# Optimization experiments

Hardware: AMD Instinct MI355X
Metric: run time of the kernel (lower is better)

## Reference

```python
import jax, jax.numpy as jnp
import numpy as np

B, L, D = 4, 2048, 512   # batch, seq_len, model_dim
H, A = 8, 64             # head_num, atten_dim (H*A == D)
EPS = 1e-5


def setup_inputs() -> dict:
    key = jax.random.key(0)
    ks = jax.random.split(key, 20)
    std = 1.0 / np.sqrt(D)
    inp = {}
    for i, name in enumerate(["Q_data", "Q_time", "K_data", "K_time", "V_time"]):
        inp[name] = jax.random.normal(ks[i], (B, L, D), dtype=jnp.float32)
    # projection params (torch Linear: y = x @ W.T + b); store as [in, out]
    for i, name in enumerate(["Wq_d", "Wq_t", "Wk_d", "Wk_t", "Wv_t", "Wo"]):
        inp[name + "_w"] = jax.random.uniform(ks[5 + i], (D, H * A), jnp.float32, -std, std)
        inp[name + "_b"] = jax.random.uniform(ks[11 + i], (H * A,), jnp.float32, -std, std)
    inp["ln_g"] = jnp.ones((D,), jnp.float32)
    inp["ln_b"] = jnp.zeros((D,), jnp.float32)
    return inp


def _proj(x, w, b):
    # [B,L,D] -> [B,H,L,A]
    y = jnp.einsum('bld,de->ble', x, w) + b
    return y.reshape(B, L, H, A).transpose(0, 2, 1, 3)


def reference(Q_data, Q_time, K_data, K_time, V_time,
              Wq_d_w, Wq_t_w, Wk_d_w, Wk_t_w, Wv_t_w, Wo_w,
              Wq_d_b, Wq_t_b, Wk_d_b, Wk_t_b, Wv_t_b, Wo_b,
              ln_g, ln_b):
    residual = Q_data
    qd = _proj(Q_data, Wq_d_w, Wq_d_b)
    qt = _proj(Q_time, Wq_t_w, Wq_t_b)
    kd = _proj(K_data, Wk_d_w, Wk_d_b)
    kt = _proj(K_time, Wk_t_w, Wk_t_b)
    vt = _proj(V_time, Wv_t_w, Wv_t_b)
    scale = 1.0 / np.sqrt(A)
    # dual QK^T scores summed before softmax
    scores = (jnp.einsum('bhqa,bhka->bhqk', qd, kd)
              + jnp.einsum('bhqa,bhka->bhqk', qt, kt)) * scale
    attn = jax.nn.softmax(scores, axis=-1)
    ctx = jnp.einsum('bhqk,bhka->bhqa', attn, vt)        # [B,H,L,A]
    ctx = ctx.transpose(0, 2, 1, 3).reshape(B, L, H * A)  # [B,L,D]
    out = jnp.einsum('bld,de->ble', ctx, Wo_w) + Wo_b
    x = out + residual
    mu = jnp.mean(x, axis=-1, keepdims=True)
    var = jnp.var(x, axis=-1, keepdims=True)
    return (x - mu) / jnp.sqrt(var + EPS) * ln_g + ln_b
```

## Files before the change

### kernel.cpp

```cpp
#include <hip/hip_runtime.h>
#include <hip/hip_bf16.h>
#include <stdint.h>


using f32x4  = __attribute__((ext_vector_type(4))) float;
using bf16x8 = __attribute__((ext_vector_type(8))) short;

typedef __attribute__((address_space(1))) const uint32_t g_u32;
typedef __attribute__((address_space(3))) uint32_t l_u32;

#if __has_builtin(__builtin_amdgcn_exp2f)
#define EXP2F __builtin_amdgcn_exp2f
#else
#define EXP2F exp2f
#endif
#define QSCALE 0.1803368801111204f

__device__ __forceinline__ void glds16(const void* g, void* l) {
  __builtin_amdgcn_global_load_lds((g_u32*)g, (l_u32*)l, 16, 0, 0);
}

__device__ __forceinline__ unsigned short f2bfu(float f) {
  __hip_bfloat16 h = __float2bfloat16(f);
  union { __hip_bfloat16 h; unsigned short u; } v;
  v.h = h;
  return v.u;
}

__device__ __forceinline__ uint32_t pack_trunc(float lo, float hi) {
  union { float f; uint32_t u; } a, b;
  a.f = lo; b.f = hi;
  return __builtin_amdgcn_perm(b.u, a.u, 0x07060302u);
}

__global__ __launch_bounds__(256) void k_prep_w(
    const float* __restrict__ w0, const float* __restrict__ w1,
    const float* __restrict__ w2, const float* __restrict__ w3,
    const float* __restrict__ w4, const float* __restrict__ w5,
    unsigned short* __restrict__ wt) {
  __shared__ float tile[64][68];
  const float* wsrc[6] = {w0, w1, w2, w3, w4, w5};
  int bid = blockIdx.x;
  int mat = bid >> 6, tid = bid & 63;
  int k0 = (tid >> 3) << 6, c0 = (tid & 7) << 6;
  const float* w = wsrc[mat];
  int t = threadIdx.x;
  {
    int r = t >> 2, cq = (t & 3) << 4;
    const float4* src = reinterpret_cast<const float4*>(w + (size_t)(k0 + r) * 512 + c0 + cq);
#pragma unroll
    for (int j = 0; j < 4; ++j) {
      float4 v = src[j];
      tile[r][cq + j * 4 + 0] = v.x;
      tile[r][cq + j * 4 + 1] = v.y;
      tile[r][cq + j * 4 + 2] = v.z;
      tile[r][cq + j * 4 + 3] = v.w;
    }
  }
  __syncthreads();
  {
    int cc = t >> 2, kq = (t & 3) << 4;
    union { unsigned short u[16]; uint4 v[2]; } p;
#pragma unroll
    for (int j = 0; j < 16; ++j) p.u[j] = f2bfu(tile[kq + j][cc]);
    unsigned short* dst = wt + (size_t)mat * 262144 + (size_t)(c0 + cc) * 512 + k0 + kq;
    *reinterpret_cast<uint4*>(dst)     = p.v[0];
    *reinterpret_cast<uint4*>(dst + 8) = p.v[1];
  }
}

__global__ __launch_bounds__(512) void k_proj2(
    const float* __restrict__ x0, const float* __restrict__ x1,
    const float* __restrict__ x2, const float* __restrict__ x3,
    const float* __restrict__ x4,
    const unsigned short* __restrict__ wt,
    const float* __restrict__ b0, const float* __restrict__ b1,
    const float* __restrict__ b2, const float* __restrict__ b3,
    const float* __restrict__ b4,
    unsigned short* __restrict__ qws, unsigned short* __restrict__ kws,
    unsigned short* __restrict__ vws) {
  __shared__ __align__(16) unsigned short Abuf[8192];
  __shared__ __align__(16) unsigned short Bbuf[2][8192];
  int bid = blockIdx.x;
  int proj = bid >> 8, rem = bid & 255;
  int cb = rem >> 6, rb = rem & 63;
  const float* xs[5] = {x0, x1, x2, x3, x4};
  const float* Ag = xs[proj] + (size_t)rb * 128 * 512;
  const unsigned short* Wg = wt + (size_t)proj * 262144 + (size_t)cb * 128 * 512;
  int t = threadIdx.x;
  int lane = t & 63, w = t >> 6, wr = w >> 2, wc = w & 3, g = lane >> 4, c = lane & 15;
  f32x4 acc[4][2];
#pragma unroll
  for (int i = 0; i < 4; ++i)
#pragma unroll
    for (int j = 0; j < 2; ++j) acc[i][j] = f32x4{0.f, 0.f, 0.f, 0.f};

  int srow[2], sch[2];
#pragma unroll
  for (int j = 0; j < 2; ++j) {
    int q = t + j * 512;
    srow[j] = q >> 3;
    sch[j] = q & 7;
  }
  float4 pa[2], pb[2];
#pragma unroll
  for (int j = 0; j < 2; ++j) {
    const float* src = Ag + (size_t)srow[j] * 512 + sch[j] * 8;
    pa[j] = *reinterpret_cast<const float4*>(src);
    pb[j] = *reinterpret_cast<const float4*>(src + 4);
  }
#pragma unroll
  for (int j = 0; j < 2; ++j) {
    int cid = t + j * 512;
    int row = cid >> 3, ch = cid & 7;
    glds16(Wg + (size_t)row * 512 + ((ch ^ (row & 7)) << 3), &Bbuf[0][cid * 8]);
  }

#pragma unroll 1
  for (int it = 0; it < 8; ++it) {
    int cur = it & 1;
    __syncthreads();
#pragma unroll
    for (int j = 0; j < 2; ++j) {
      union { unsigned short u[8]; uint4 v; } p;
      p.u[0] = f2bfu(pa[j].x); p.u[1] = f2bfu(pa[j].y);
      p.u[2] = f2bfu(pa[j].z); p.u[3] = f2bfu(pa[j].w);
      p.u[4] = f2bfu(pb[j].x); p.u[5] = f2bfu(pb[j].y);
      p.u[6] = f2bfu(pb[j].z); p.u[7] = f2bfu(pb[j].w);
      *reinterpret_cast<uint4*>(&Abuf[srow[j] * 64 + ((sch[j] ^ (srow[j] & 7)) << 3)]) = p.v;
    }
    __syncthreads();
    if (it < 7) {
#pragma unroll
      for (int j = 0; j < 2; ++j) {
        const float* src = Ag + (size_t)srow[j] * 512 + (it + 1) * 64 + sch[j] * 8;
        pa[j] = *reinterpret_cast<const float4*>(src);
        pb[j] = *reinterpret_cast<const float4*>(src + 4);
      }
#pragma unroll
      for (int j = 0; j < 2; ++j) {
        int cid = t + j * 512;
        int row = cid >> 3, ch = cid & 7;
        glds16(Wg + (size_t)row * 512 + (it + 1) * 64 + ((ch ^ (row & 7)) << 3),
               &Bbuf[cur ^ 1][cid * 8]);
      }
    }
#pragma unroll
    for (int fi = 0; fi < 2; ++fi) {
      bf16x8 af[4], bfr[2];
#pragma unroll
      for (int mi = 0; mi < 4; ++mi) {
        int arow = wr * 64 + mi * 16 + c;
        af[mi] = *reinterpret_cast<const bf16x8*>(
            &Abuf[arow * 64 + (((fi * 4 + g) ^ (arow & 7)) << 3)]);
      }
#pragma unroll
      for (int ni = 0; ni < 2; ++ni) {
        int brow = wc * 32 + ni * 16 + c;
        bfr[ni] = *reinterpret_cast<const bf16x8*>(
            &Bbuf[cur][brow * 64 + (((fi * 4 + g) ^ (brow & 7)) << 3)]);
      }
      __builtin_amdgcn_s_setprio(1);
#pragma unroll
      for (int mi = 0; mi < 4; ++mi)
#pragma unroll
        for (int ni = 0; ni < 2; ++ni)
          acc[mi][ni] = __builtin_amdgcn_mfma_f32_16x16x32_bf16(af[mi], bfr[ni], acc[mi][ni], 0, 0, 0);
      __builtin_amdgcn_s_setprio(0);
    }
  }

  const float* bias_arr[5] = {b0, b1, b2, b3, b4};
  const float* bias = bias_arr[proj];
  float scale = (proj < 2) ? QSCALE : 1.0f;
  unsigned short* qkdst = (proj < 2) ? qws : kws;
  int half = (proj & 1) ? 64 : 0;
#pragma unroll
  for (int ni = 0; ni < 2; ++ni) {
    int n = wc * 32 + ni * 16 + c;
    int h = cb * 2 + (n >> 6);
    int a = n & 63;
    float bv = bias[cb * 128 + n];
#pragma unroll
    for (int mi = 0; mi < 4; ++mi) {
#pragma unroll
      for (int rr = 0; rr < 4; ++rr) {
        float v = (acc[mi][ni][rr] + bv) * scale;
        unsigned short u = f2bfu(v);
        int rowg = rb * 128 + wr * 64 + mi * 16 + g * 4 + rr;
        int b = rowg >> 11, l = rowg & 2047;
        if (proj < 4) {
          qkdst[((size_t)(b * 8 + h) * 2048 + l) * 128 + half + a] = u;
        } else {
          vws[((size_t)(b * 8 + h) * 64 + a) * 2048 + l] = u;
        }
      }
    }
  }
}

__device__ __forceinline__ void gemm_core(
    const unsigned short* Ag, const unsigned short* Wg,
    unsigned short* Al, unsigned short* Bl, f32x4 acc[4]) {
  int t = threadIdx.x;
  int lane = t & 63, w = t >> 6, g = lane >> 4, c = lane & 15;
#pragma unroll 1
  for (int it = 0; it < 8; ++it) {
    __syncthreads();
#pragma unroll
    for (int j = 0; j < 2; ++j) {
      int cid = t + j * 256;
      int row = cid >> 3, ch = cid & 7;
      glds16(Ag + (size_t)row * 512 + it * 64 + ((ch ^ (row & 7)) << 3), Al + cid * 8);
      glds16(Wg + (size_t)row * 512 + it * 64 + ((ch ^ (row & 7)) << 3), Bl + cid * 8);
    }
    __syncthreads();
#pragma unroll
    for (int fi = 0; fi < 2; ++fi) {
      int arow = w * 16 + c;
      bf16x8 af = *reinterpret_cast<const bf16x8*>(
          Al + arow * 64 + (((fi * 4 + g) ^ (arow & 7)) << 3));
#pragma unroll
      for (int ct = 0; ct < 4; ++ct) {
        int brow = ct * 16 + c;
        bf16x8 bf = *reinterpret_cast<const bf16x8*>(
            Bl + brow * 64 + (((fi * 4 + g) ^ (brow & 7)) << 3));
        acc[ct] = __builtin_amdgcn_mfma_f32_16x16x32_bf16(af, bf, acc[ct], 0, 0, 0);
      }
    }
  }
}

__global__ __launch_bounds__(256) void k_attn(
    const unsigned short* __restrict__ qws, const unsigned short* __restrict__ kws,
    const unsigned short* __restrict__ vws, unsigned short* __restrict__ ctxb) {
  __shared__ __align__(16) unsigned short Kb[2][8192];
  __shared__ __align__(16) unsigned short Vb[2][4096];
  __shared__ __align__(16) unsigned short Pl[4][2][1152];
  int orig = blockIdx.x;
  int xcd = orig & 7, j = orig >> 3;
  int bh = xcd * 4 + (j >> 4), qb = j & 15;
  int t = threadIdx.x;
  int w = t >> 6, lane = t & 63, g = lane >> 4, c = lane & 15;

  const unsigned short* Kg = kws + (size_t)bh * 2048 * 128;
  const unsigned short* Vg = vws + (size_t)bh * 64 * 2048;

  bf16x8 qf[2][4];
#pragma unroll
  for (int qt = 0; qt < 2; ++qt) {
    const unsigned short* Qg =
        qws + ((size_t)bh * 2048 + qb * 128 + w * 32 + qt * 16 + c) * 128;
#pragma unroll
    for (int fi = 0; fi < 4; ++fi)
      qf[qt][fi] = *reinterpret_cast<const bf16x8*>(Qg + fi * 32 + g * 8);
  }

  f32x4 o[2][4];
#pragma unroll
  for (int qt = 0; qt < 2; ++qt)
#pragma unroll
    for (int at = 0; at < 4; ++at) o[qt][at] = f32x4{0.f, 0.f, 0.f, 0.f};
  float lsum[2] = {0.f, 0.f};
  char* Pw0 = reinterpret_cast<char*>(&Pl[w][0][0]) + c * 144;
  char* Pw1 = reinterpret_cast<char*>(&Pl[w][1][0]) + c * 144;

#pragma unroll
  for (int jj = 0; jj < 4; ++jj) {
    int cid = t + jj * 256;
    int row = cid >> 4, ch = cid & 15;
    glds16(Kg + (size_t)row * 128 + ((ch ^ (row & 15)) << 3), &Kb[0][cid * 8]);
  }
#pragma unroll
  for (int jj = 0; jj < 2; ++jj) {
    int cid = t + jj * 256;
    int a = cid >> 3, ch = cid & 7;
    glds16(Vg + (size_t)a * 2048 + ((ch ^ (a & 7)) << 3), &Vb[0][cid * 8]);
  }
  __syncthreads();

#pragma unroll 1
  for (int it = 0; it < 32; ++it) {
    int cur = it & 1;
    if (it < 31) {
      int nxt = cur ^ 1;
#pragma unroll
      for (int jj = 0; jj < 4; ++jj) {
        int cid = t + jj * 256;
        int row = cid >> 4, ch = cid & 15;
        glds16(Kg + ((size_t)(it + 1) * 64 + row) * 128 + ((ch ^ (row & 15)) << 3),
               &Kb[nxt][cid * 8]);
      }
#pragma unroll
      for (int jj = 0; jj < 2; ++jj) {
        int cid = t + jj * 256;
        int a = cid >> 3, ch = cid & 7;
        glds16(Vg + (size_t)a * 2048 + (it + 1) * 64 + ((ch ^ (a & 7)) << 3),
               &Vb[nxt][cid * 8]);
      }
    }

    f32x4 s[2][4];
#pragma unroll
    for (int qt = 0; qt < 2; ++qt)
#pragma unroll
      for (int mt = 0; mt < 4; ++mt) s[qt][mt] = f32x4{0.f, 0.f, 0.f, 0.f};
#pragma unroll
    for (int fi = 0; fi < 4; ++fi) {
      bf16x8 kf[4];
#pragma unroll
      for (int mt = 0; mt < 4; ++mt)
        kf[mt] = *reinterpret_cast<const bf16x8*>(
            &Kb[cur][(mt * 16 + c) * 128 + (((fi * 4 + g) ^ c) << 3)]);
      __builtin_amdgcn_s_setprio(1);
#pragma unroll
      for (int mt = 0; mt < 4; ++mt) {
        s[0][mt] = __builtin_amdgcn_mfma_f32_16x16x32_bf16(kf[mt], qf[0][fi], s[0][mt], 0, 0, 0);
        s[1][mt] = __builtin_amdgcn_mfma_f32_16x16x32_bf16(kf[mt], qf[1][fi], s[1][mt], 0, 0, 0);
      }
      __builtin_amdgcn_s_setprio(0);
    }

    bf16x8 vf0[4], vf1[4];
#pragma unroll
    for (int at = 0; at < 4; ++at) {
      int arow = at * 16 + c;
      vf0[at] = *reinterpret_cast<const bf16x8*>(
          &Vb[cur][arow * 64 + ((g ^ (c & 7)) << 3)]);
      vf1[at] = *reinterpret_cast<const bf16x8*>(
          &Vb[cur][arow * 64 + (((4 + g) ^ (c & 7)) << 3)]);
    }

#pragma unroll
    for (int qt = 0; qt < 2; ++qt) {
      char* Pw = qt ? Pw1 : Pw0;
      float ls = 0.f;
#pragma unroll
      for (int mt = 0; mt < 4; ++mt) {
        float p0 = EXP2F(s[qt][mt][0]);
        float p1 = EXP2F(s[qt][mt][1]);
        float p2 = EXP2F(s[qt][mt][2]);
        float p3 = EXP2F(s[qt][mt][3]);
        ls += (p0 + p1) + (p2 + p3);
        uint2 pk;
        pk.x = pack_trunc(p0, p1);
        pk.y = pack_trunc(p2, p3);
        *reinterpret_cast<uint2*>(Pw + mt * 32 + g * 8) = pk;
      }
      lsum[qt] += ls;
    }

#pragma unroll
    for (int qt = 0; qt < 2; ++qt) {
      char* Pw = qt ? Pw1 : Pw0;
      bf16x8 pf0 = *reinterpret_cast<const bf16x8*>(Pw + g * 16);
      bf16x8 pf1 = *reinterpret_cast<const bf16x8*>(Pw + 64 + g * 16);
      __builtin_amdgcn_s_setprio(1);
#pragma unroll
      for (int at = 0; at < 4; ++at) {
        o[qt][at] = __builtin_amdgcn_mfma_f32_16x16x32_bf16(pf0, vf0[at], o[qt][at], 0, 0, 0);
        o[qt][at] = __builtin_amdgcn_mfma_f32_16x16x32_bf16(pf1, vf1[at], o[qt][at], 0, 0, 0);
      }
      __builtin_amdgcn_s_setprio(0);
    }
    __syncthreads();
  }

  int b = bh >> 3, h = bh & 7;
#pragma unroll
  for (int qt = 0; qt < 2; ++qt) {
    lsum[qt] += __shfl_xor(lsum[qt], 16);
    lsum[qt] += __shfl_xor(lsum[qt], 32);
    float rinv[4];
#pragma unroll
    for (int r = 0; r < 4; ++r) rinv[r] = 1.0f / __shfl(lsum[qt], g * 4 + r);
    int rowg0 = b * 2048 + qb * 128 + w * 32 + qt * 16 + g * 4;
#pragma unroll
    for (int at = 0; at < 4; ++at)
#pragma unroll
      for (int r = 0; r < 4; ++r) {
        float v = o[qt][at][r] * rinv[r];
        ctxb[(size_t)(rowg0 + r) * 512 + h * 64 + at * 16 + c] = f2bfu(v);
      }
  }
}

__global__ __launch_bounds__(256) void k_oproj(
    const unsigned short* __restrict__ ctxb, const unsigned short* __restrict__ wt,
    const float* __restrict__ bo, const float* __restrict__ resid,
    float* __restrict__ out) {
  __shared__ __align__(16) unsigned short Al[4096];
  __shared__ __align__(16) unsigned short Bl[4096];
  int bid = blockIdx.x;
  int rb = bid >> 3, cb = bid & 7;
  const unsigned short* Ag = ctxb + (size_t)rb * 64 * 512;
  const unsigned short* Wg = wt + (size_t)5 * 262144 + (size_t)cb * 64 * 512;
  f32x4 acc[4];
#pragma unroll
  for (int i = 0; i < 4; ++i) acc[i] = f32x4{0.f, 0.f, 0.f, 0.f};
  gemm_core(Ag, Wg, Al, Bl, acc);
  int lane = threadIdx.x & 63, w = threadIdx.x >> 6, g = lane >> 4, c = lane & 15;
  int rowbase = rb * 64 + w * 16 + g * 4;
#pragma unroll
  for (int ct = 0; ct < 4; ++ct) {
    int n = cb * 64 + ct * 16 + c;
    float bv = bo[n];
#pragma unroll
    for (int r = 0; r < 4; ++r) {
      int rowg = rowbase + r;
      size_t di = (size_t)rowg * 512 + n;
      out[di] = acc[ct][r] + bv + resid[di];
    }
  }
}

__global__ __launch_bounds__(256) void k_ln(float* __restrict__ out,
                                            const float* __restrict__ gam,
                                            const float* __restrict__ bet) {
  int row = blockIdx.x * 4 + (threadIdx.x >> 6);
  int lane = threadIdx.x & 63;
  float* x = out + (size_t)row * 512 + lane * 8;
  float4 v0 = reinterpret_cast<const float4*>(x)[0];
  float4 v1 = reinterpret_cast<const float4*>(x)[1];
  float s = v0.x + v0.y + v0.z + v0.w + v1.x + v1.y + v1.z + v1.w;
  float q = v0.x * v0.x + v0.y * v0.y + v0.z * v0.z + v0.w * v0.w +
            v1.x * v1.x + v1.y * v1.y + v1.z * v1.z + v1.w * v1.w;
#pragma unroll
  for (int d = 1; d < 64; d <<= 1) {
    s += __shfl_xor(s, d);
    q += __shfl_xor(q, d);
  }
  float mu = s * (1.0f / 512.0f);
  float var = q * (1.0f / 512.0f) - mu * mu;
  float rstd = rsqrtf(var + 1e-5f);
  float4 g0 = reinterpret_cast<const float4*>(gam + lane * 8)[0];
  float4 g1 = reinterpret_cast<const float4*>(gam + lane * 8)[1];
  float4 b0 = reinterpret_cast<const float4*>(bet + lane * 8)[0];
  float4 b1 = reinterpret_cast<const float4*>(bet + lane * 8)[1];
  v0.x = (v0.x - mu) * rstd * g0.x + b0.x;
  v0.y = (v0.y - mu) * rstd * g0.y + b0.y;
  v0.z = (v0.z - mu) * rstd * g0.z + b0.z;
  v0.w = (v0.w - mu) * rstd * g0.w + b0.w;
  v1.x = (v1.x - mu) * rstd * g1.x + b1.x;
  v1.y = (v1.y - mu) * rstd * g1.y + b1.y;
  v1.z = (v1.z - mu) * rstd * g1.z + b1.z;
  v1.w = (v1.w - mu) * rstd * g1.w + b1.w;
  reinterpret_cast<float4*>(x)[0] = v0;
  reinterpret_cast<float4*>(x)[1] = v1;
}

extern "C" void kernel_launch(void* const* d_in, const int* in_sizes, int n_in,
                              void* d_out, int out_size, void* d_ws, size_t ws_size,
                              hipStream_t stream) {
  const float* Qd  = (const float*)d_in[0];
  const float* Qt  = (const float*)d_in[1];
  const float* Kd  = (const float*)d_in[2];
  const float* Kt  = (const float*)d_in[3];
  const float* Vt  = (const float*)d_in[4];
  const float* Wqd = (const float*)d_in[5];
  const float* bqd = (const float*)d_in[6];
  const float* Wqt = (const float*)d_in[7];
  const float* bqt = (const float*)d_in[8];
  const float* Wkd = (const float*)d_in[9];
  const float* bkd = (const float*)d_in[10];
  const float* Wkt = (const float*)d_in[11];
  const float* bkt = (const float*)d_in[12];
  const float* Wvt = (const float*)d_in[13];
  const float* bvt = (const float*)d_in[14];
  const float* Wo  = (const float*)d_in[15];
  const float* bo  = (const float*)d_in[16];
  const float* lng = (const float*)d_in[17];
  const float* lnb = (const float*)d_in[18];

  char* ws = (char*)d_ws;
  unsigned short* wt   = (unsigned short*)(ws);
  unsigned short* qws  = (unsigned short*)(ws + 3145728);
  unsigned short* kws  = (unsigned short*)(ws + 19922944);
  unsigned short* vws  = (unsigned short*)(ws + 36700160);
  unsigned short* ctxb = (unsigned short*)(ws + 45088768);
  float* out = (float*)d_out;

  k_prep_w<<<384, 256, 0, stream>>>(Wqd, Wqt, Wkd, Wkt, Wvt, Wo, wt);
  k_proj2<<<1280, 512, 0, stream>>>(Qd, Qt, Kd, Kt, Vt, wt,
                                    bqd, bqt, bkd, bkt, bvt, qws, kws, vws);
  k_attn<<<512, 256, 0, stream>>>(qws, kws, vws, ctxb);
  k_oproj<<<1024, 256, 0, stream>>>(ctxb, wt, bo, Qd, out);
  k_ln<<<2048, 256, 0, stream>>>(out, lng, lnb);
}
```

Measured before the change: 135.1 us.

## Keep softmax probabilities in registers and permute V fragment loads to match

Removes the per-wave LDS staging buffer for the exponentiated scores. The packed bf16 probabilities now feed the PV MFMA straight from registers. To make the register layout of P line up with the MFMA k-index, the V operand is gathered from LDS as permuted 8-byte pieces. This saves an LDS write/read round trip per tile and some LDS capacity, but doubles the number of smaller V loads from LDS.

```diff
diff --git a/kernel.cpp b/kernel.cpp
--- a/kernel.cpp
+++ b/kernel.cpp
@@ -236,7 +236,6 @@
     const unsigned short* __restrict__ vws, unsigned short* __restrict__ ctxb) {
   __shared__ __align__(16) unsigned short Kb[2][8192];
   __shared__ __align__(16) unsigned short Vb[2][4096];
-  __shared__ __align__(16) unsigned short Pl[4][2][1152];
   int orig = blockIdx.x;
   int xcd = orig & 7, j = orig >> 3;
   int bh = xcd * 4 + (j >> 4), qb = j & 15;
@@ -262,8 +261,6 @@
 #pragma unroll
     for (int at = 0; at < 4; ++at) o[qt][at] = f32x4{0.f, 0.f, 0.f, 0.f};
   float lsum[2] = {0.f, 0.f};
-  char* Pw0 = reinterpret_cast<char*>(&Pl[w][0][0]) + c * 144;
-  char* Pw1 = reinterpret_cast<char*>(&Pl[w][1][0]) + c * 144;
 
 #pragma unroll
   for (int jj = 0; jj < 4; ++jj) {
@@ -321,19 +318,9 @@
       __builtin_amdgcn_s_setprio(0);
     }
 
-    bf16x8 vf0[4], vf1[4];
-#pragma unroll
-    for (int at = 0; at < 4; ++at) {
-      int arow = at * 16 + c;
-      vf0[at] = *reinterpret_cast<const bf16x8*>(
-          &Vb[cur][arow * 64 + ((g ^ (c & 7)) << 3)]);
-      vf1[at] = *reinterpret_cast<const bf16x8*>(
-          &Vb[cur][arow * 64 + (((4 + g) ^ (c & 7)) << 3)]);
-    }
-
+    uint32_t pku[2][4][2];
 #pragma unroll
     for (int qt = 0; qt < 2; ++qt) {
-      char* Pw = qt ? Pw1 : Pw0;
       float ls = 0.f;
 #pragma unroll
       for (int mt = 0; mt < 4; ++mt) {
@@ -342,24 +329,41 @@
         float p2 = EXP2F(s[qt][mt][2]);
         float p3 = EXP2F(s[qt][mt][3]);
         ls += (p0 + p1) + (p2 + p3);
-        uint2 pk;
-        pk.x = pack_trunc(p0, p1);
-        pk.y = pack_trunc(p2, p3);
-        *reinterpret_cast<uint2*>(Pw + mt * 32 + g * 8) = pk;
+        pku[qt][mt][0] = pack_trunc(p0, p1);
+        pku[qt][mt][1] = pack_trunc(p2, p3);
       }
       lsum[qt] += ls;
     }
 
+    union u32x4_bf { uint32_t u[4]; bf16x8 v; };
+    u32x4_bf pf[2][2];
 #pragma unroll
     for (int qt = 0; qt < 2; ++qt) {
-      char* Pw = qt ? Pw1 : Pw0;
-      bf16x8 pf0 = *reinterpret_cast<const bf16x8*>(Pw + g * 16);
-      bf16x8 pf1 = *reinterpret_cast<const bf16x8*>(Pw + 64 + g * 16);
+      pf[qt][0].u[0] = pku[qt][0][0]; pf[qt][0].u[1] = pku[qt][0][1];
+      pf[qt][0].u[2] = pku[qt][1][0]; pf[qt][0].u[3] = pku[qt][1][1];
+      pf[qt][1].u[0] = pku[qt][2][0]; pf[qt][1].u[1] = pku[qt][2][1];
+      pf[qt][1].u[2] = pku[qt][3][0]; pf[qt][1].u[3] = pku[qt][3][1];
+    }
+#pragma unroll
+    for (int at = 0; at < 4; ++at) {
+      int arow = at * 16 + c;
+      u32x4_bf vf0, vf1;
+#pragma unroll
+      for (int pp = 0; pp < 2; ++pp) {
+        int ch0 = (2 * pp + (g >> 1)) ^ (arow & 7);
+        int ch1 = (4 + 2 * pp + (g >> 1)) ^ (arow & 7);
+        uint2 d0 = *reinterpret_cast<const uint2*>(
+            &Vb[cur][arow * 64 + ch0 * 8 + ((g & 1) << 2)]);
+        uint2 d1 = *reinterpret_cast<const uint2*>(
+            &Vb[cur][arow * 64 + ch1 * 8 + ((g & 1) << 2)]);
+        vf0.u[2 * pp] = d0.x; vf0.u[2 * pp + 1] = d0.y;
+        vf1.u[2 * pp] = d1.x; vf1.u[2 * pp + 1] = d1.y;
+      }
       __builtin_amdgcn_s_setprio(1);
 #pragma unroll
-      for (int at = 0; at < 4; ++at) {
-        o[qt][at] = __builtin_amdgcn_mfma_f32_16x16x32_bf16(pf0, vf0[at], o[qt][at], 0, 0, 0);
-        o[qt][at] = __builtin_amdgcn_mfma_f32_16x16x32_bf16(pf1, vf1[at], o[qt][at], 0, 0, 0);
+      for (int qt = 0; qt < 2; ++qt) {
+        o[qt][at] = __builtin_amdgcn_mfma_f32_16x16x32_bf16(pf[qt][0].v, vf0.v, o[qt][at], 0, 0, 0);
+        o[qt][at] = __builtin_amdgcn_mfma_f32_16x16x32_bf16(pf[qt][1].v, vf1.v, o[qt][at], 0, 0, 0);
       }
       __builtin_amdgcn_s_setprio(0);
     }
```

After: 133.2 us. About the same (-1.3%).
